# Kernel optimization log

Measured on AMD Instinct MI355X. Metric: run time of the kernel, lower is better.

Reference implementation:

```python
import jax, jax.numpy as jnp
import numpy as np

# dims: batch, seq (<=300 due to tril buffer), raw embed, model dim (hardcoded 300), experts, heads, head_size
B, T, D_IN, D, E, H, HS = 64, 300, 768, 300, 8, 4, 16
TOP_K = E // 2


def setup_inputs() -> dict:
    key = jax.random.key(0)
    ks = jax.random.split(key, 10)
    f = lambda k, s, sc: jax.random.normal(k, s, jnp.float32) * sc
    return {
        "x": jax.random.normal(ks[0], (B, T, D_IN), jnp.float32),
        "wh_bias": jnp.zeros((D_IN,), jnp.float32),
        "wh_W": f(ks[1], (D, D_IN), 0.02),              # WhitenLayer linear (no bias)
        "Wq": f(ks[2], (H, HS, D), 0.05),                # stacked per-head query weights
        "Wk": f(ks[3], (H, HS, D), 0.05),
        "Wv": f(ks[4], (H, HS, D), 0.05),
        "proj_W": f(ks[5], (D, H * HS), 0.05),
        "proj_b": jnp.zeros((D,), jnp.float32),
        "exp_W1": f(ks[6], (E, 2 * D, D), (2.0 / (2 * D)) ** 0.5),  # kaiming fan_out
        "exp_b1": jnp.zeros((E, 2 * D), jnp.float32),
        "exp_W2": f(ks[7], (E, D, 2 * D), (2.0 / D) ** 0.5),
        "exp_b2": jnp.zeros((E, D), jnp.float32),
        "w_gate": f(ks[8], (D, E), 0.02),
    }


def reference(x, wh_bias, wh_W, Wq, Wk, Wv, proj_W, proj_b,
              exp_W1, exp_b1, exp_W2, exp_b2, w_gate):
    # WhitenLayer: lin(x - bias)  (dropout identity in eval)
    xw = jnp.einsum('btd,od->bto', x - wh_bias, wh_W)          # [B,T,D]

    # MultiHeadAttention (causal, scale = C**-0.5 with C = D = 300)
    q = jnp.einsum('btd,hkd->bhtk', xw, Wq)
    k = jnp.einsum('btd,hkd->bhtk', xw, Wk)
    v = jnp.einsum('btd,hkd->bhtk', xw, Wv)
    wei = jnp.einsum('bhtk,bhsk->bhts', q, k) * (D ** -0.5)
    tril = jnp.tril(jnp.ones((T, T), bool))
    wei = jax.nn.softmax(jnp.where(tril, wei, -jnp.inf), axis=-1)
    att = jnp.einsum('bhts,bhsk->bthk', wei, v).reshape(x.shape[0], T, H * HS)
    xa = att @ proj_W.T + proj_b                               # [B,T,D]

    # noisy_top_k_gating in eval mode (no noise); masked dispatch == dense weighted sum
    logits = xa @ w_gate                                       # [B,T,E]
    topv, topi = jax.lax.top_k(logits, TOP_K)
    sel = jax.nn.one_hot(topi, E, dtype=bool).any(axis=-2)     # [B,T,E] top-k mask
    sparse = jnp.where(sel, logits, -jnp.inf)
    gprob = jax.nn.softmax(sparse, axis=-1)                    # zero on non-selected

    # all experts applied densely (forward also recomputes them all anyway)
    h = jax.nn.relu(jnp.einsum('btd,ehd->bteh', xa, exp_W1) + exp_b1)
    eo = jnp.einsum('bteh,eoh->bteo', h, exp_W2) + exp_b2      # [B,T,E,D]

    gates = jnp.einsum('bte,bteo->bto', gprob, eo)             # dispatched mixture [B,T,D]
    # forward: (gates.unsqueeze(-2) * expert_outputs).sum(-2) == gates * sum_e expert_e
    return gates * eo.sum(axis=-2)
```

## Files before the change

### kernel.cpp

```cpp
#include <hip/hip_runtime.h>
#include <cstdint>
#include <cstddef>

#define B_   64
#define T_   300
#define DIN_ 768
#define D_   300
#define E_   8
#define NTOK (B_*T_)

typedef __attribute__((ext_vector_type(8))) short bf8_t;
typedef __attribute__((ext_vector_type(4))) float f4_t;

__device__ __forceinline__ unsigned short f2bf(float v) {
  union { float f; unsigned u; } a; a.f = v;
  unsigned r = a.u + 0x7fff + ((a.u >> 16) & 1);
  return (unsigned short)(r >> 16);
}
__device__ __forceinline__ float bf2f(unsigned short s) {
  union { float f; unsigned u; } a; a.u = ((unsigned)s) << 16; return a.f;
}
__device__ __forceinline__ void split3(float v, unsigned short& p0,
                                       unsigned short& p1, unsigned short& p2) {
  p0 = f2bf(v);
  float r1 = v - bf2f(p0);
  p1 = f2bf(r1);
  float r2 = r1 - bf2f(p1);
  p2 = f2bf(r2);
}
__device__ __forceinline__ void split2(float v, unsigned short& p0,
                                       unsigned short& p1) {
  p0 = f2bf(v);
  p1 = f2bf(v - bf2f(p0));
}

__device__ __forceinline__ void gld16(const unsigned short* g, unsigned short* l) {
  __builtin_amdgcn_global_load_lds(
      (const __attribute__((address_space(1))) unsigned int*)g,
      (__attribute__((address_space(3))) unsigned int*)l, 16, 0, 0);
}

__global__ void biasproj_kernel(const float* __restrict__ wh_bias,
                                const float* __restrict__ wh_W,
                                float* __restrict__ bp) {
  int o = blockIdx.x * blockDim.x + threadIdx.x;
  if (o >= D_) return;
  float acc = 0.f;
  const float* row = wh_W + (size_t)o * DIN_;
  for (int d = 0; d < DIN_; ++d) acc += wh_bias[d] * row[d];
  bp[o] = -acc;
}

__global__ void split_pad(const float* __restrict__ src, unsigned short* __restrict__ dst,
                          int rows, int K, int Kp, size_t planeStride, int np) {
  int n = rows * Kp;
  for (int i = blockIdx.x * blockDim.x + threadIdx.x; i < n; i += gridDim.x * blockDim.x) {
    int r = i / Kp, c = i % Kp;
    unsigned short p0 = 0, p1 = 0, p2 = 0;
    if (c < K) split3(src[(size_t)r * K + c], p0, p1, p2);
    dst[i] = p0;
    dst[planeStride + i] = p1;
    if (np == 3) dst[2 * planeStride + i] = p2;
  }
}

template<int AFP, int EPI, int JN, int WM, int NP, int NPO, int SWZ>
__global__ __launch_bounds__(WM * 64) void mfma_gen(
    const void* __restrict__ Av, size_t aPStride, int ldA,
    const unsigned short* __restrict__ Bg, size_t bPStride,
    const float* __restrict__ bias, float* __restrict__ C,
    unsigned short* __restrict__ Po, size_t poStride, int ldPo,
    float* __restrict__ gsum, float* __restrict__ esum,
    const float* __restrict__ gate,
    int M, int N, int K) {
  constexpr int TILE_M = WM * 32;
  constexpr int BROWS  = JN * 32;
  constexpr int APB    = TILE_M * 64;
  constexpr int BPB    = BROWS * 64;
  constexpr int AINSTS = NP * APB / 1024;
  constexpr int BINSTS = NP * BPB / 1024;
  static_assert(!AFP || NP == 3, "AFP path writes 3 planes");
  __shared__ unsigned short Ap[NP][TILE_M * 32];
  __shared__ unsigned short Bp[NP][BROWS * 32];
  const int tid = threadIdx.x;
  int bxv = blockIdx.x, byv = blockIdx.y;
  if constexpr (SWZ) {
    const int nx  = gridDim.x;
    const int nwg = nx * gridDim.y;
    const int id  = byv * nx + bxv;
    const int xcd = id & 7, idx = id >> 3;
    const int q = nwg >> 3, r = nwg & 7;
    const int nid = (xcd < r) ? (xcd * (q + 1) + idx)
                              : (r * (q + 1) + (xcd - r) * q + idx);
    bxv = nid % nx;
    byv = nid / nx;
  }
  const int bm = byv * TILE_M, bn = bxv * BROWS;
  const int widx = tid >> 6;
  const int wr = (widx >> 1) * 64;
  const int wc = (widx & 1) * (JN * 16);
  const int lane = tid & 63;
  const int lr = lane & 15;
  const int kg = lane >> 4;
  const int sw = (lr >> 1) & 3;
  const int Kp = (K + 31) & ~31;
  const int arow = tid >> 1, ahalf = (tid & 1) * 16;
  const int asw = (arow >> 1) & 3;

  auto stageB = [&](int k0) {
    for (int q = widx; q < BINSTS; q += WM) {
      const int f   = q * 1024 + lane * 16;
      const int pp  = f / BPB;
      const int rem = f % BPB;
      const int row = rem >> 6;
      const int cl  = ((rem >> 4) & 3) ^ ((row >> 1) & 3);
      int brow = bn + row; if (brow >= N) brow = N - 1;
      gld16(Bg + (size_t)pp * bPStride + (size_t)brow * Kp + k0 + cl * 8,
            (unsigned short*)Bp + q * 512);
    }
  };
  auto stageA = [&](int k0) {
    if constexpr (AFP) {
      const float* Arow = (const float*)Av + (size_t)(bm + arow) * ldA + k0 + ahalf;
      #pragma unroll
      for (int u = 0; u < 4; ++u) {
        float4 qv = *(const float4*)&Arow[u * 4];
        float vv[4] = {qv.x, qv.y, qv.z, qv.w};
        unsigned short s0[4], s1[4], s2[4];
        #pragma unroll
        for (int w = 0; w < 4; ++w) split3(vv[w], s0[w], s1[w], s2[w]);
        const int k  = ahalf + u * 4;
        const int so = arow * 32 + (((k >> 3) ^ asw) << 3) + (k & 7);
        *(unsigned*)&Ap[0][so]     = (unsigned)s0[0] | ((unsigned)s0[1] << 16);
        *(unsigned*)&Ap[0][so + 2] = (unsigned)s0[2] | ((unsigned)s0[3] << 16);
        *(unsigned*)&Ap[1][so]     = (unsigned)s1[0] | ((unsigned)s1[1] << 16);
        *(unsigned*)&Ap[1][so + 2] = (unsigned)s1[2] | ((unsigned)s1[3] << 16);
        *(unsigned*)&Ap[2][so]     = (unsigned)s2[0] | ((unsigned)s2[1] << 16);
        *(unsigned*)&Ap[2][so + 2] = (unsigned)s2[2] | ((unsigned)s2[3] << 16);
      }
    } else {
      for (int q = widx; q < AINSTS; q += WM) {
        const int f   = q * 1024 + lane * 16;
        const int pp  = f / APB;
        const int rem = f % APB;
        const int row = rem >> 6;
        const int cl  = ((rem >> 4) & 3) ^ ((row >> 1) & 3);
        gld16((const unsigned short*)Av + (size_t)pp * aPStride +
                  (size_t)(bm + row) * Kp + k0 + cl * 8,
              (unsigned short*)Ap + q * 512);
      }
    }
  };

  f4_t acc[4][JN];
  #pragma unroll
  for (int i = 0; i < 4; ++i)
    #pragma unroll
    for (int j = 0; j < JN; ++j) acc[i][j] = (f4_t){0.f, 0.f, 0.f, 0.f};

  stageB(0); stageA(0);
  __syncthreads();
  for (int k0 = 0; k0 < Kp; k0 += 32) {
    bf8_t a[4][NP], b[JN][NP];
    #pragma unroll
    for (int i = 0; i < 4; ++i)
      #pragma unroll
      for (int p = 0; p < NP; ++p)
        a[i][p] = *(const bf8_t*)&Ap[p][(wr + i * 16 + lr) * 32 + ((kg ^ sw) << 3)];
    #pragma unroll
    for (int j = 0; j < JN; ++j)
      #pragma unroll
      for (int p = 0; p < NP; ++p)
        b[j][p] = *(const bf8_t*)&Bp[p][(wc + j * 16 + lr) * 32 + ((kg ^ sw) << 3)];
    __syncthreads();
    if (k0 + 32 < Kp) { stageB(k0 + 32); stageA(k0 + 32); }
    #pragma unroll
    for (int i = 0; i < 4; ++i)
      #pragma unroll
      for (int j = 0; j < JN; ++j) {
        f4_t c = acc[i][j];
        if constexpr (NP == 3) {
          c = __builtin_amdgcn_mfma_f32_16x16x32_bf16(a[i][2], b[j][0], c, 0, 0, 0);
          c = __builtin_amdgcn_mfma_f32_16x16x32_bf16(a[i][1], b[j][1], c, 0, 0, 0);
          c = __builtin_amdgcn_mfma_f32_16x16x32_bf16(a[i][0], b[j][2], c, 0, 0, 0);
          c = __builtin_amdgcn_mfma_f32_16x16x32_bf16(a[i][1], b[j][0], c, 0, 0, 0);
          c = __builtin_amdgcn_mfma_f32_16x16x32_bf16(a[i][0], b[j][1], c, 0, 0, 0);
          c = __builtin_amdgcn_mfma_f32_16x16x32_bf16(a[i][0], b[j][0], c, 0, 0, 0);
        } else {
          c = __builtin_amdgcn_mfma_f32_16x16x32_bf16(a[i][1], b[j][0], c, 0, 0, 0);
          c = __builtin_amdgcn_mfma_f32_16x16x32_bf16(a[i][0], b[j][1], c, 0, 0, 0);
          c = __builtin_amdgcn_mfma_f32_16x16x32_bf16(a[i][0], b[j][0], c, 0, 0, 0);
        }
        acc[i][j] = c;
      }
    __syncthreads();
  }
  #pragma unroll
  for (int i = 0; i < 4; ++i) {
    #pragma unroll
    for (int r = 0; r < 4; ++r) {
      const int row = bm + wr + i * 16 + kg * 4 + r;
      float g = 0.f;
      if constexpr (EPI >= 2 && EPI <= 4) g = gate[(size_t)row * E_];
      #pragma unroll
      for (int j = 0; j < JN; ++j) {
        const int col = bn + wc + j * 16 + lr;
        float v = acc[i][j][r];
        if constexpr (EPI == 0) {
          if (col < N) {
            if (bias) v += bias[col];
            C[(size_t)row * N + col] = v;
          }
        } else if constexpr (EPI == 1 || EPI == 5 || EPI == 6) {
          if (col < ldPo) {
            unsigned short p0 = 0, p1 = 0, p2 = 0;
            if (col < N) {
              v += bias[col];
              if constexpr (EPI == 1) v = fmaxf(v, 0.f);
              if constexpr (EPI == 6) C[(size_t)row * N + col] = v;
              if constexpr (NPO == 3) split3(v, p0, p1, p2);
              else                    split2(v, p0, p1);
            }
            size_t o = (size_t)row * ldPo + col;
            Po[o] = p0;
            Po[poStride + o] = p1;
            if constexpr (NPO == 3) Po[2 * poStride + o] = p2;
          }
        } else {
          if (col < N) {
            float eo = v + bias[col];
            size_t idx = (size_t)row * N + col;
            if constexpr (EPI == 2) {
              gsum[idx] = g * eo;
              esum[idx] = eo;
            } else if constexpr (EPI == 3) {
              gsum[idx] += g * eo;
              esum[idx] += eo;
            } else {
              float gs = gsum[idx] + g * eo;
              float es = esum[idx] + eo;
              C[idx] = gs * es;
            }
          }
        }
      }
    }
  }
}

__global__ __launch_bounds__(64) void attn_kernel(
    const float* __restrict__ qkv, float* __restrict__ attout) {
  const int bt = blockIdx.x;
  const int b = bt / T_, t = bt % T_;
  const int lane = threadIdx.x;
  const int h = lane >> 4, li = lane & 15;
  __shared__ float p[4][304];
  const float scale = rsqrtf((float)D_);
  const float* qrow = qkv + (size_t)bt * 192 + h * 16;
  const float4 q0 = *(const float4*)(qrow);
  const float4 q1 = *(const float4*)(qrow + 4);
  const float4 q2 = *(const float4*)(qrow + 8);
  const float4 q3 = *(const float4*)(qrow + 12);
  const float* kb0 = qkv + (size_t)b * T_ * 192 + 64 + h * 16;
  float mmax = -1e30f;
  for (int s = li; s <= t; s += 16) {
    const float* kr = kb0 + (size_t)s * 192;
    float4 k0 = *(const float4*)(kr);
    float4 k1 = *(const float4*)(kr + 4);
    float4 k2 = *(const float4*)(kr + 8);
    float4 k3 = *(const float4*)(kr + 12);
    float acc = q0.x * k0.x + q0.y * k0.y + q0.z * k0.z + q0.w * k0.w;
    acc += q1.x * k1.x + q1.y * k1.y + q1.z * k1.z + q1.w * k1.w;
    acc += q2.x * k2.x + q2.y * k2.y + q2.z * k2.z + q2.w * k2.w;
    acc += q3.x * k3.x + q3.y * k3.y + q3.z * k3.z + q3.w * k3.w;
    acc *= scale;
    p[h][s] = acc;
    mmax = fmaxf(mmax, acc);
  }
  #pragma unroll
  for (int m = 8; m >= 1; m >>= 1) mmax = fmaxf(mmax, __shfl_xor(mmax, m, 16));
  float lsum = 0.f;
  for (int s = li; s <= t; s += 16) {
    float e = __expf(p[h][s] - mmax);
    p[h][s] = e;
    lsum += e;
  }
  #pragma unroll
  for (int m = 8; m >= 1; m >>= 1) lsum += __shfl_xor(lsum, m, 16);
  const float inv = 1.0f / lsum;
  const float* vcol = qkv + (size_t)b * T_ * 192 + 128 + h * 16 + li;
  float o0 = 0.f, o1 = 0.f, o2 = 0.f, o3 = 0.f;
  const int s4 = (t + 1) & ~3;
  int s = 0;
  for (; s < s4; s += 4) {
    float4 pw = *(const float4*)&p[h][s];
    o0 += pw.x * vcol[(size_t)s * 192];
    o1 += pw.y * vcol[(size_t)(s + 1) * 192];
    o2 += pw.z * vcol[(size_t)(s + 2) * 192];
    o3 += pw.w * vcol[(size_t)(s + 3) * 192];
  }
  for (; s <= t; ++s) o0 += p[h][s] * vcol[(size_t)s * 192];
  attout[(size_t)bt * 192 + lane] = ((o0 + o1) + (o2 + o3)) * inv;
}

__global__ void logits_kernel(const float* __restrict__ xa,
                              const float* __restrict__ w_gate,
                              float* __restrict__ logits) {
  int idx = blockIdx.x * blockDim.x + threadIdx.x;
  if (idx >= NTOK * E_) return;
  int n = idx >> 3, e = idx & 7;
  const float* xr = xa + (size_t)n * D_;
  float acc = 0.f;
  for (int d = 0; d < D_; ++d) acc += xr[d] * w_gate[(size_t)d * E_ + e];
  logits[idx] = acc;
}

__global__ void gate_kernel(const float* __restrict__ logits,
                            float* __restrict__ gprob) {
  int n = blockIdx.x * blockDim.x + threadIdx.x;
  if (n >= NTOK) return;
  float l[E_];
  #pragma unroll
  for (int e = 0; e < E_; ++e) l[e] = logits[(size_t)n * E_ + e];
  bool sel[E_] = {false, false, false, false, false, false, false, false};
  for (int kk = 0; kk < E_ / 2; ++kk) {
    int bi = -1; float bv = -1e38f;
    #pragma unroll
    for (int e = 0; e < E_; ++e)
      if (!sel[e] && l[e] > bv) { bv = l[e]; bi = e; }
    sel[bi] = true;
  }
  float mx = -1e38f;
  #pragma unroll
  for (int e = 0; e < E_; ++e) if (sel[e]) mx = fmaxf(mx, l[e]);
  float s = 0.f, pp[E_];
  #pragma unroll
  for (int e = 0; e < E_; ++e) {
    pp[e] = sel[e] ? __expf(l[e] - mx) : 0.f;
    s += pp[e];
  }
  float inv = 1.0f / s;
  #pragma unroll
  for (int e = 0; e < E_; ++e) gprob[(size_t)n * E_ + e] = pp[e] * inv;
}

extern "C" void kernel_launch(void* const* d_in, const int* in_sizes, int n_in,
                              void* d_out, int out_size, void* d_ws, size_t ws_size,
                              hipStream_t stream) {
  const float* x       = (const float*)d_in[0];
  const float* wh_bias = (const float*)d_in[1];
  const float* wh_W    = (const float*)d_in[2];
  const float* Wq      = (const float*)d_in[3];
  const float* Wk      = (const float*)d_in[4];
  const float* Wv      = (const float*)d_in[5];
  const float* proj_W  = (const float*)d_in[6];
  const float* proj_b  = (const float*)d_in[7];
  const float* exp_W1  = (const float*)d_in[8];
  const float* exp_b1  = (const float*)d_in[9];
  const float* exp_W2  = (const float*)d_in[10];
  const float* exp_b2  = (const float*)d_in[11];
  const float* w_gate  = (const float*)d_in[12];
  (void)in_sizes; (void)n_in; (void)out_size;

  char* ws = (char*)d_ws;
  size_t off = 0;
  auto alloc = [&](size_t bytes) {
    void* p = ws + off; off = (off + bytes + 255) & ~(size_t)255; return p;
  };
  typedef unsigned short us;
  float* bp    = (float*)alloc(300 * 4);
  us* whp      = (us*)alloc((size_t)3 * 300 * 768 * 2);
  us* qkvp     = (us*)alloc((size_t)2 * 192 * 320 * 2);
  us* projp    = (us*)alloc((size_t)3 * 300 * 64 * 2);
  us* w1p      = (us*)alloc((size_t)2 * 4800 * 320 * 2);
  us* w2p      = (us*)alloc(((size_t)2 * 2400 * 608 + 64 * 608) * 2);
  float* gprob = (float*)alloc((size_t)NTOK * E_ * 4);
  us* xwreg    = (us*)alloc((size_t)2 * NTOK * 320 * 2);
  float* qkvb  = (float*)alloc((size_t)NTOK * 192 * 4);
  us* xap      = (us*)alloc((size_t)2 * NTOK * 320 * 2);

  float* xa = (float*)xwreg;

  const size_t xp3Bytes  = (size_t)3 * NTOK * DIN_ * 2;
  const size_t hplBytes  = (size_t)2 * NTOK * 608 * 2;
  const size_t esumBytes = (size_t)NTOK * 300 * 4;
  const size_t hplAl = (hplBytes + 255) & ~(size_t)255;
  int CHe;
  us* hpl;
  float* esum;
  us* xp3 = nullptr;
  bool preX = false;
  if (off + xp3Bytes <= ws_size) {
    char* region = ws + off;
    off += (xp3Bytes + 255) & ~(size_t)255;
    xp3  = (us*)region;
    hpl  = (us*)region;
    esum = (float*)(region + hplAl);
    CHe  = NTOK;
    preX = true;
  } else if (off + hplBytes + esumBytes <= ws_size) {
    hpl  = (us*)alloc(hplBytes);
    esum = (float*)alloc(esumBytes);
    CHe  = NTOK;
  } else {
    hpl  = xwreg;
    esum = qkvb;
    CHe  = 9600;
  }

  biasproj_kernel<<<2, 256, 0, stream>>>(wh_bias, wh_W, bp);
  auto SP = [&](const float* s, us* dbase, int rows, int K, int Kp, size_t pstr, int np) {
    int n = rows * Kp;
    int g = (n + 255) / 256; if (g > 4096) g = 4096;
    split_pad<<<g, 256, 0, stream>>>(s, dbase, rows, K, Kp, pstr, np);
  };
  SP(wh_W,   whp,              300,  768, 768, (size_t)300 * 768, 3);
  SP(Wq,     qkvp,             64,   300, 320, (size_t)192 * 320, 2);
  SP(Wk,     qkvp + 64 * 320,  64,   300, 320, (size_t)192 * 320, 2);
  SP(Wv,     qkvp + 128 * 320, 64,   300, 320, (size_t)192 * 320, 2);
  SP(proj_W, projp,            300,  64,  64,  (size_t)300 * 64, 3);
  SP(exp_W1, w1p,              4800, 300, 320, (size_t)4800 * 320, 2);
  SP(exp_W2, w2p,              2400, 600, 608, (size_t)2400 * 608, 2);

  if (preX) {
    SP(x, xp3, NTOK, DIN_, DIN_, (size_t)NTOK * DIN_, 3);
    dim3 g(5, NTOK / 128);
    mfma_gen<0, 5, 2, 4, 3, 2, 1><<<g, 256, 0, stream>>>(
        xp3, (size_t)NTOK * DIN_, 0, whp, (size_t)300 * 768, bp, nullptr,
        xwreg, (size_t)NTOK * 320, 320, nullptr, nullptr, nullptr,
        NTOK, D_, DIN_);
  } else {
    dim3 g(5, NTOK / 128);
    mfma_gen<1, 5, 2, 4, 3, 2, 1><<<g, 256, 0, stream>>>(
        x, 0, DIN_, whp, (size_t)300 * 768, bp, nullptr,
        xwreg, (size_t)NTOK * 320, 320, nullptr, nullptr, nullptr,
        NTOK, D_, DIN_);
  }
  {
    dim3 g(3, NTOK / 128);
    mfma_gen<0, 0, 2, 4, 2, 2, 1><<<g, 256, 0, stream>>>(
        xwreg, (size_t)NTOK * 320, 0, qkvp, (size_t)192 * 320, nullptr, qkvb,
        nullptr, 0, 0, nullptr, nullptr, nullptr,
        NTOK, 192, D_);
  }
  attn_kernel<<<NTOK, 64, 0, stream>>>(qkvb, qkvb);

  {
    dim3 g(5, NTOK / 128);
    mfma_gen<1, 6, 2, 4, 3, 2, 1><<<g, 256, 0, stream>>>(
        qkvb, 0, 192, projp, (size_t)300 * 64, proj_b, xa,
        xap, (size_t)NTOK * 320, 320, nullptr, nullptr, nullptr,
        NTOK, D_, 64);
  }
  logits_kernel<<<(NTOK * E_ + 255) / 256, 256, 0, stream>>>(xa, w_gate, gprob);
  gate_kernel<<<(NTOK + 255) / 256, 256, 0, stream>>>(gprob, gprob);

  for (int c = 0; c < NTOK / CHe; ++c) {
    const int tok0 = c * CHe;
    float* gsum = (float*)d_out + (size_t)tok0 * D_;
    dim3 g1(5, CHe / 128);
    dim3 g2(5, CHe / 128);
    for (int e = 0; e < E_; ++e) {
      const us* w1e = w1p + (size_t)e * 600 * 320;
      const us* w2e = w2p + (size_t)e * 300 * 608;
      const float* bb1 = exp_b1 + (size_t)e * 600;
      const float* bb2 = exp_b2 + (size_t)e * D_;
      const float* gate = gprob + (size_t)tok0 * E_ + e;
      mfma_gen<0, 1, 4, 4, 2, 2, 1><<<g1, 256, 0, stream>>>(
          xap + (size_t)tok0 * 320, (size_t)NTOK * 320, 0,
          w1e, (size_t)4800 * 320, bb1, nullptr,
          hpl, (size_t)CHe * 608, 608, nullptr, nullptr, nullptr,
          CHe, 600, D_);
      if (e == 0)
        mfma_gen<0, 2, 2, 4, 2, 2, 1><<<g2, 256, 0, stream>>>(
            hpl, (size_t)CHe * 608, 0, w2e, (size_t)2400 * 608, bb2, nullptr,
            nullptr, 0, 0, gsum, esum, gate, CHe, D_, 600);
      else if (e < E_ - 1)
        mfma_gen<0, 3, 2, 4, 2, 2, 1><<<g2, 256, 0, stream>>>(
            hpl, (size_t)CHe * 608, 0, w2e, (size_t)2400 * 608, bb2, nullptr,
            nullptr, 0, 0, gsum, esum, gate, CHe, D_, 600);
      else
        mfma_gen<0, 4, 2, 4, 2, 2, 1><<<g2, 256, 0, stream>>>(
            hpl, (size_t)CHe * 608, 0, w2e, (size_t)2400 * 608, bb2,
            (float*)d_out + (size_t)tok0 * D_,
            nullptr, 0, 0, gsum, esum, gate, CHe, D_, 600);
    }
  }
}
```

Before: 988.2 us.

## Tile causal attention over query rows with LDS-staged K/V chunks

The attention kernel now assigns 10 query rows of one batch to each block, one wavefront per row, instead of one wavefront per block. K and V are loaded cooperatively into shared memory in chunks of 32 keys, so every staged key and value row is reused by all 10 queries in the block rather than fetched from global memory once per query. In exchange it adds block-wide barriers around every chunk and uses a large shared-memory footprint for the per-row probability buffers, which may limit occupancy. Causal imbalance inside a block leaves some wavefronts idle while the last row finishes its chunks.

New measurement: 989.5 us. About the same (+0.1%).

```diff
diff --git a/kernel.cpp b/kernel.cpp
--- a/kernel.cpp
+++ b/kernel.cpp
@@ -8,6 +8,8 @@
 #define D_   300
 #define E_   8
 #define NTOK (B_*T_)
+#define TW   10
+#define SC   32
 
 typedef __attribute__((ext_vector_type(8))) short bf8_t;
 typedef __attribute__((ext_vector_type(4))) float f4_t;
@@ -248,59 +250,88 @@
   }
 }
 
-__global__ __launch_bounds__(64) void attn_kernel(
+__global__ __launch_bounds__(64 * TW) void attn_kernel(
     const float* __restrict__ qkv, float* __restrict__ attout) {
-  const int bt = blockIdx.x;
-  const int b = bt / T_, t = bt % T_;
-  const int lane = threadIdx.x;
+  const int nch_blk = T_ / TW;
+  const int b   = blockIdx.x / nch_blk;
+  const int tch = blockIdx.x % nch_blk;
+  const int w    = threadIdx.x >> 6;
+  const int lane = threadIdx.x & 63;
   const int h = lane >> 4, li = lane & 15;
-  __shared__ float p[4][304];
+  const int t    = tch * TW + w;
+  const int tmax = tch * TW + TW - 1;
+  __shared__ float kv[SC][68];
+  __shared__ float p[TW][4][304];
   const float scale = rsqrtf((float)D_);
-  const float* qrow = qkv + (size_t)bt * 192 + h * 16;
+  const float* base = qkv + (size_t)b * T_ * 192;
+  const float* qrow = base + (size_t)t * 192 + h * 16;
   const float4 q0 = *(const float4*)(qrow);
   const float4 q1 = *(const float4*)(qrow + 4);
   const float4 q2 = *(const float4*)(qrow + 8);
   const float4 q3 = *(const float4*)(qrow + 12);
-  const float* kb0 = qkv + (size_t)b * T_ * 192 + 64 + h * 16;
+  const int nch = tmax / SC + 1;
+
   float mmax = -1e30f;
-  for (int s = li; s <= t; s += 16) {
-    const float* kr = kb0 + (size_t)s * 192;
-    float4 k0 = *(const float4*)(kr);
-    float4 k1 = *(const float4*)(kr + 4);
-    float4 k2 = *(const float4*)(kr + 8);
-    float4 k3 = *(const float4*)(kr + 12);
-    float acc = q0.x * k0.x + q0.y * k0.y + q0.z * k0.z + q0.w * k0.w;
-    acc += q1.x * k1.x + q1.y * k1.y + q1.z * k1.z + q1.w * k1.w;
-    acc += q2.x * k2.x + q2.y * k2.y + q2.z * k2.z + q2.w * k2.w;
-    acc += q3.x * k3.x + q3.y * k3.y + q3.z * k3.z + q3.w * k3.w;
-    acc *= scale;
-    p[h][s] = acc;
-    mmax = fmaxf(mmax, acc);
+  for (int c = 0; c < nch; ++c) {
+    const int s0 = c * SC;
+    __syncthreads();
+    for (int i = threadIdx.x; i < SC * 16; i += 64 * TW) {
+      const int r = i >> 4, c4 = (i & 15) * 4;
+      int sr = s0 + r; if (sr > T_ - 1) sr = T_ - 1;
+      *(float4*)&kv[r][c4] = *(const float4*)&base[(size_t)sr * 192 + 64 + c4];
+    }
+    __syncthreads();
+    const int send = (s0 + SC - 1 < t) ? s0 + SC - 1 : t;
+    for (int s = s0 + li; s <= send; s += 16) {
+      const float* kr = &kv[s - s0][h * 16];
+      float4 k0 = *(const float4*)(kr);
+      float4 k1 = *(const float4*)(kr + 4);
+      float4 k2 = *(const float4*)(kr + 8);
+      float4 k3 = *(const float4*)(kr + 12);
+      float acc = q0.x * k0.x + q0.y * k0.y + q0.z * k0.z + q0.w * k0.w;
+      acc += q1.x * k1.x + q1.y * k1.y + q1.z * k1.z + q1.w * k1.w;
+      acc += q2.x * k2.x + q2.y * k2.y + q2.z * k2.z + q2.w * k2.w;
+      acc += q3.x * k3.x + q3.y * k3.y + q3.z * k3.z + q3.w * k3.w;
+      acc *= scale;
+      p[w][h][s] = acc;
+      mmax = fmaxf(mmax, acc);
+    }
   }
   #pragma unroll
   for (int m = 8; m >= 1; m >>= 1) mmax = fmaxf(mmax, __shfl_xor(mmax, m, 16));
   float lsum = 0.f;
   for (int s = li; s <= t; s += 16) {
-    float e = __expf(p[h][s] - mmax);
-    p[h][s] = e;
+    float e = __expf(p[w][h][s] - mmax);
+    p[w][h][s] = e;
     lsum += e;
   }
   #pragma unroll
   for (int m = 8; m >= 1; m >>= 1) lsum += __shfl_xor(lsum, m, 16);
   const float inv = 1.0f / lsum;
-  const float* vcol = qkv + (size_t)b * T_ * 192 + 128 + h * 16 + li;
+
   float o0 = 0.f, o1 = 0.f, o2 = 0.f, o3 = 0.f;
-  const int s4 = (t + 1) & ~3;
-  int s = 0;
-  for (; s < s4; s += 4) {
-    float4 pw = *(const float4*)&p[h][s];
-    o0 += pw.x * vcol[(size_t)s * 192];
-    o1 += pw.y * vcol[(size_t)(s + 1) * 192];
-    o2 += pw.z * vcol[(size_t)(s + 2) * 192];
-    o3 += pw.w * vcol[(size_t)(s + 3) * 192];
-  }
-  for (; s <= t; ++s) o0 += p[h][s] * vcol[(size_t)s * 192];
-  attout[(size_t)bt * 192 + lane] = ((o0 + o1) + (o2 + o3)) * inv;
+  for (int c = 0; c < nch; ++c) {
+    const int s0 = c * SC;
+    __syncthreads();
+    for (int i = threadIdx.x; i < SC * 16; i += 64 * TW) {
+      const int r = i >> 4, c4 = (i & 15) * 4;
+      int sr = s0 + r; if (sr > T_ - 1) sr = T_ - 1;
+      *(float4*)&kv[r][c4] = *(const float4*)&base[(size_t)sr * 192 + 128 + c4];
+    }
+    __syncthreads();
+    const int send = (s0 + SC - 1 < t) ? s0 + SC - 1 : t;
+    const int col = h * 16 + li;
+    int s = s0;
+    for (; s + 3 <= send; s += 4) {
+      float4 pw = *(const float4*)&p[w][h][s];
+      o0 += pw.x * kv[s - s0][col];
+      o1 += pw.y * kv[s + 1 - s0][col];
+      o2 += pw.z * kv[s + 2 - s0][col];
+      o3 += pw.w * kv[s + 3 - s0][col];
+    }
+    for (; s <= send; ++s) o0 += p[w][h][s] * kv[s - s0][col];
+  }
+  attout[((size_t)b * T_ + t) * 192 + lane] = ((o0 + o1) + (o2 + o3)) * inv;
 }
 
 __global__ void logits_kernel(const float* __restrict__ xa,
@@ -443,7 +474,7 @@
         nullptr, 0, 0, nullptr, nullptr, nullptr,
         NTOK, 192, D_);
   }
-  attn_kernel<<<NTOK, 64, 0, stream>>>(qkvb, qkvb);
+  attn_kernel<<<B_ * (T_ / TW), 64 * TW, 0, stream>>>(qkvb, qkvb);
 
   {
     dim3 g(5, NTOK / 128);
```
